# Kernel tuning notes

Measured on AMD Instinct MI355X. Metric: run time of the kernel, lower is better.

Reference implementation:

```python
import jax, jax.numpy as jnp
import numpy as np

# Irreps 0e+1o+2e+3o: (name, dim); total irreps dim D = 1+3+5+7 = 16
IRS = [("0e", 1), ("1o", 3), ("2e", 5), ("3o", 7)]
D = 16
# path multiplicities per correlation order (MACE-like)
MULS = {3: [5, 8, 10, 10], 2: [2, 3, 4, 4], 1: [1, 1, 1, 1]}
NUM_RBF = 32
CHANNELS = 128
NUM_SPECIES = 64
BATCH = 256


def _make_U():
    # Sparse Clebsch-Gordan-like basis tensors: shape (D,)*order + (mul, ir_dim).
    # Stand-in for e3nn.reduced_symmetric_tensor_product_basis: deterministic,
    rng = np.random.default_rng(42)
    U = {}
    for order in (3, 2, 1):
        for (ir, dim), mul in zip(IRS, MULS[order]):
            shape = (D,) * order + (mul, dim)
            dense = rng.standard_normal(shape).astype(np.float32)
            mask = (rng.random(shape) < 0.1).astype(np.float32)
            U[(order, ir)] = jnp.asarray(dense * mask)
    return U

U_BASIS = _make_U()
WKEYS = [(o, ir) for o in (3, 2, 1) for ir, _ in IRS]


def setup_inputs() -> dict:
    key = jax.random.key(0)
    ks = jax.random.split(key, 16)
    inp = {
        "x": jax.random.normal(ks[0], (BATCH, CHANNELS, D), dtype=jnp.float32),
        "index": jax.random.randint(ks[1], (BATCH,), 0, NUM_SPECIES),
        "embed_table": jax.random.normal(ks[2], (NUM_SPECIES, NUM_RBF), dtype=jnp.float32),
    }
    i = 3
    for order in (3, 2, 1):
        for (ir, _), mul in zip(IRS, MULS[order]):
            inp[f"w{order}_{ir}"] = jax.random.normal(ks[i], (NUM_RBF, mul, CHANNELS), dtype=jnp.float32)
            i += 1
    return inp


def _forward(x, species_ind, Wd):
    # x: (b, c, D); species_ind: (b, num_rbf); Wd[(order, ir)]: (num_rbf, mul, c)
    out = {}
    fresh = set()
    for order in (3, 2, 1):
        for ir, _ in IRS:
            u = U_BASIS[(order, ir)] / order  # ((D,)*order, mul, ir_dim)
            # species-gathered per-channel path weights: (b, mul, c)
            w = jnp.einsum('be,ekc->bkc', species_ind, Wd[(order, ir)])
            if ir not in out:
                # highest order: contract one D axis with x, mul with w
                out[ir] = jnp.einsum('...jki,bkc,bcj->bc...i', u, w, x)
                fresh.add(ir)
            else:
                out[ir] = out[ir] + jnp.einsum('...ki,bkc->bc...i', u, w)
        for ir, _ in IRS:
            if ir in fresh:
                fresh.discard(ir)
                continue
            # contract one more D axis against x after each lower order
            out[ir] = jnp.einsum('bc...ji,bcj->bc...i', out[ir], x)
    # final per-ir shape (b, c, ir_dim); concat -> (b, c, D)
    return jnp.concatenate([out[ir] for ir, _ in IRS], axis=-1)


def reference(x, index, embed_table, w3_0e, w3_1o, w3_2e, w3_3o, w2_0e, w2_1o, w2_2e, w2_3o, w1_0e, w1_1o, w1_2e, w1_3o):
    ws = (w3_0e, w3_1o, w3_2e, w3_3o, w2_0e, w2_1o, w2_2e, w2_3o, w1_0e, w1_1o, w1_2e, w1_3o)
    Wd = {k: w for k, w in zip(WKEYS, ws)}
    species_ind = embed_table[index]  # (b, num_rbf) embedding lookup
    return _forward(x, species_ind, Wd)
```

## Files before the change

kernel.cpp:

```cpp
#include <hip/hip_runtime.h>
#include <cstdint>
#include <cmath>
#include <cstring>

#define D16    16
#define CH     128
#define NBATCH 256
#define NSP    64
#define NRBF   32
#define NKK    50
#define NT3    816
#define NT2    136
#define LD3    160
#define LD2    64
#define U3_FLOATS (NT3*LD3)
#define U2_FLOATS (NT2*LD2)
#define U1_FLOATS 256
#define U_TOTAL   (U3_FLOATS+U2_FLOATS+U1_FLOATS)

#define KPAD   1024
#define NPAD   256

typedef __attribute__((ext_vector_type(8)))  short short8;
typedef __attribute__((ext_vector_type(16))) float f32x16;

__device__ uint16_t g_B[NPAD*KPAD];
__device__ float    g_ws[NSP*NKK*CH];

__device__ __constant__ int8_t KK_ARR[NKK] = {
  0,0,0,0,0, 1,1,1,1,1,1,1,1, 2,2,2,2,2,2,2,2,2,2, 3,3,3,3,3,3,3,3,3,3,
  4,4, 5,5,5, 6,6,6,6, 7,7,7,7, 8,9,10,11 };
__device__ __constant__ int8_t KK_K[NKK] = {
  0,1,2,3,4, 0,1,2,3,4,5,6,7, 0,1,2,3,4,5,6,7,8,9, 0,1,2,3,4,5,6,7,8,9,
  0,1, 0,1,2, 0,1,2,3, 0,1,2,3, 0,0,0,0 };
__device__ __constant__ int8_t ARR_MUL[12] = {5,8,10,10, 2,3,4,4, 1,1,1,1};

struct WPtrs { const float* p[12]; };

struct TTab { uint8_t a0[KPAD]; uint8_t a1[KPAD]; uint8_t a2[KPAD]; };
constexpr TTab make_tab() {
  TTab t{};
  int i = 0;
  for (int A = 0; A < 16; ++A)
    for (int B = A; B < 16; ++B)
      for (int C = B; C < 16; ++C) { t.a0[i]=(uint8_t)A; t.a1[i]=(uint8_t)B; t.a2[i]=(uint8_t)C; ++i; }
  for (int A = 0; A < 16; ++A)
    for (int B = A; B < 16; ++B) { t.a0[i]=(uint8_t)A; t.a1[i]=(uint8_t)B; t.a2[i]=16; ++i; }
  for (int A = 0; A < 16; ++A) { t.a0[i]=(uint8_t)A; t.a1[i]=16; t.a2[i]=16; ++i; }
  for (; i < KPAD; ++i) { t.a0[i]=17; t.a1[i]=17; t.a2[i]=17; }
  return t;
}
static constexpr TTab TT = make_tab();

template<int K>
__device__ __forceinline__ float featK(const float (&xv)[16]) {
  constexpr int A = TT.a0[K], B = TT.a1[K], C = TT.a2[K];
  if constexpr (A == 17) { return 0.f; }
  else {
    float m = xv[A];
    if constexpr (B < 16) m *= xv[B];
    if constexpr (C < 16) m *= xv[C];
    return m;
  }
}

template<int K0>
__device__ __forceinline__ uint32_t pack2(const float (&xv)[16]) {
  if constexpr (TT.a0[K0] == 17 && TT.a0[K0+1] == 17) { return 0u; }
  else {
    float lo = featK<K0>(xv);
    float hi = featK<K0+1>(xv);
    uint32_t d;
    asm("v_cvt_pk_bf16_f32 %0, %1, %2" : "=v"(d) : "v"(lo), "v"(hi));
    return d;
  }
}

template<int CHUNK>
__device__ __forceinline__ short8 build_frag(const float (&xv)[16], bool kg_hi) {
  uint32_t pk0 = pack2<CHUNK*16 + 0>(xv);
  uint32_t pk1 = pack2<CHUNK*16 + 2>(xv);
  uint32_t pk2 = pack2<CHUNK*16 + 4>(xv);
  uint32_t pk3 = pack2<CHUNK*16 + 6>(xv);
  uint32_t pk4 = pack2<CHUNK*16 + 8>(xv);
  uint32_t pk5 = pack2<CHUNK*16 + 10>(xv);
  uint32_t pk6 = pack2<CHUNK*16 + 12>(xv);
  uint32_t pk7 = pack2<CHUNK*16 + 14>(xv);
  union { uint32_t u[4]; short8 s; } r;
  r.u[0] = kg_hi ? pk4 : pk0;
  r.u[1] = kg_hi ? pk5 : pk1;
  r.u[2] = kg_hi ? pk6 : pk2;
  r.u[3] = kg_hi ? pk7 : pk3;
  return r.s;
}

__device__ uint32_t colpack(int cc) {
  int kk, ii;
  if (cc < 149) {
    if (cc < 5)       { kk = cc;               ii = 0; }
    else if (cc < 29) { int r = cc-5;  kk = 5  + r/3; ii = 1 + r%3; }
    else if (cc < 79) { int r = cc-29; kk = 13 + r/5; ii = 4 + r%5; }
    else              { int r = cc-79; kk = 23 + r/7; ii = 9 + r%7; }
  } else if (cc < 208) {
    int j = cc - 149;
    if (j < 2)        { kk = 33 + j;           ii = 0; }
    else if (j < 11)  { int r = j-2;  kk = 35 + r/3; ii = 1 + r%3; }
    else if (j < 31)  { int r = j-11; kk = 38 + r/5; ii = 4 + r%5; }
    else              { int r = j-31; kk = 42 + r/7; ii = 9 + r%7; }
  } else {
    int j = cc - 208;
    if (j < 1)        { kk = 46; ii = 0; }
    else if (j < 4)   { kk = 47; ii = j; }
    else if (j < 9)   { kk = 48; ii = j; }
    else              { kk = 49; ii = j; }
  }
  return (uint32_t)((kk<<4) | ii);
}

__global__ void weights_kernel(const float* __restrict__ embed, WPtrs wp) {
  int kk = blockIdx.x;
  int s  = blockIdx.y;
  int c  = threadIdx.x;
  int ai = KK_ARR[kk];
  int k  = KK_K[kk];
  int mul = ARR_MUL[ai];
  const float* __restrict__ W = wp.p[ai];
  float a = 0.f;
  #pragma unroll 8
  for (int e = 0; e < NRBF; ++e)
    a = fmaf(embed[s*NRBF + e], W[(e*mul + k)*CH + c], a);
  g_ws[(s*NKK + kk)*CH + c] = a;
}

__global__ __launch_bounds__(512) void main_kernel(const float* __restrict__ x,
                                                   const int* __restrict__ index,
                                                   float* __restrict__ out) {
  __shared__ uint16_t Bbuf[2][4][2][256][8];
  __shared__ float    out_lds[128*18];
  __shared__ uint32_t tab2[256];

  const int tid  = threadIdx.x;
  const int lane = tid & 63;
  const int l31  = lane & 31;
  const int kg   = lane >> 5;
  const bool kg_hi = (kg != 0);
  const int w    = tid >> 6;
  const int wm   = w >> 1;
  const int wn   = w & 1;
  const int b    = blockIdx.x;
  const int s    = index[b];

  const int row = wm*32 + l31;
  float xv[16];
  {
    const float4* xs = (const float4*)(x + ((size_t)b*CH + row)*D16);
    #pragma unroll
    for (int qq = 0; qq < 4; ++qq) {
      float4 v = xs[qq];
      xv[qq*4+0]=v.x; xv[qq*4+1]=v.y; xv[qq*4+2]=v.z; xv[qq*4+3]=v.w;
    }
  }

  for (int i = tid; i < 128*18; i += 512) out_lds[i] = 0.f;
  if (tid < 256) tab2[tid] = (tid < 224) ? colpack(tid) : 0u;

  #pragma unroll
  for (int q = 0; q < 4; ++q) {
    uint4 v = *(const uint4*)(g_B + ((size_t)q*512 + tid)*8);
    *(uint4*)((char*)&Bbuf[0][q][0][0][0] + tid*16) = v;
  }
  __syncthreads();

  f32x16 acc[4];
  #pragma unroll
  for (int nt = 0; nt < 4; ++nt)
    #pragma unroll
    for (int q = 0; q < 16; ++q) acc[nt][q] = 0.f;

  uint4 bpre[4];

#define DO_CHUNK(CC, CB) { \
    short8 af = build_frag<(CC)>(xv, kg_hi); \
    _Pragma("unroll") \
    for (int nt = 0; nt < 4; ++nt) { \
      short8 bf = *(const short8*)&Bbuf[(CB)][(CC)&3][kg][wn*128 + nt*32 + l31][0]; \
      acc[nt] = __builtin_amdgcn_mfma_f32_32x32x16_bf16(af, bf, acc[nt], 0, 0, 0); \
    } }

#define DO_STAGE(S) { \
    if ((S) < 15) { \
      _Pragma("unroll") \
      for (int q = 0; q < 4; ++q) \
        bpre[q] = *(const uint4*)(g_B + ((size_t)(((S)+1)*4+q)*512 + tid)*8); \
    } \
    DO_CHUNK((S)*4+0, (S)&1) \
    DO_CHUNK((S)*4+1, (S)&1) \
    DO_CHUNK((S)*4+2, (S)&1) \
    DO_CHUNK((S)*4+3, (S)&1) \
    if ((S) < 15) { \
      _Pragma("unroll") \
      for (int q = 0; q < 4; ++q) \
        *(uint4*)((char*)&Bbuf[((S)+1)&1][q][0][0][0] + tid*16) = bpre[q]; \
    } \
    __syncthreads(); }

  DO_STAGE(0)  DO_STAGE(1)  DO_STAGE(2)  DO_STAGE(3)
  DO_STAGE(4)  DO_STAGE(5)  DO_STAGE(6)  DO_STAGE(7)
  DO_STAGE(8)  DO_STAGE(9)  DO_STAGE(10) DO_STAGE(11)
  DO_STAGE(12) DO_STAGE(13) DO_STAGE(14) DO_STAGE(15)

#undef DO_STAGE
#undef DO_CHUNK

  #pragma unroll
  for (int nt = 0; nt < 4; ++nt) {
    int col = wn*128 + nt*32 + l31;
    if (col < 224) {
      uint32_t v = tab2[col];
      int kk = v >> 4, ii = v & 15;
      const float* wsrow = g_ws + ((size_t)s*NKK + kk)*CH + wm*32;
      #pragma unroll
      for (int qg = 0; qg < 4; ++qg) {
        int rlb = 8*qg + 4*kg;
        float4 wv = *(const float4*)(wsrow + rlb);
        atomicAdd(&out_lds[(wm*32 + rlb + 0)*18 + ii], wv.x * acc[nt][qg*4+0]);
        atomicAdd(&out_lds[(wm*32 + rlb + 1)*18 + ii], wv.y * acc[nt][qg*4+1]);
        atomicAdd(&out_lds[(wm*32 + rlb + 2)*18 + ii], wv.z * acc[nt][qg*4+2]);
        atomicAdd(&out_lds[(wm*32 + rlb + 3)*18 + ii], wv.w * acc[nt][qg*4+3]);
      }
    }
  }
  __syncthreads();

  { int cch = tid >> 2, q = tid & 3;
    float4 o;
    o.x = out_lds[cch*18 + q*4 + 0];
    o.y = out_lds[cch*18 + q*4 + 1];
    o.z = out_lds[cch*18 + q*4 + 2];
    o.w = out_lds[cch*18 + q*4 + 3];
    *(float4*)(out + ((size_t)b*CH + cch)*D16 + q*4) = o; }
}

namespace host_rng {

typedef unsigned __int128 u128;

static inline u128 pcg_mult() {
  return (((u128)0x2360ed051fc65da4ULL) << 64) | 0x4385df649fccf645ULL;
}

struct PCG {
  u128 state, inc;
  inline uint64_t next() {
    state = state * pcg_mult() + inc;
    uint64_t hi = (uint64_t)(state >> 64), lo = (uint64_t)state;
    uint64_t x = hi ^ lo;
    unsigned rot = (unsigned)(hi >> 58);
    return (x >> rot) | (x << ((64u - rot) & 63u));
  }
  inline double nextd() { return (double)(next() >> 11) * (1.0 / 9007199254740992.0); }
};

static inline uint32_t hashmix(uint32_t v, uint32_t& hc) {
  v ^= hc; hc *= 0x931e8875u; v *= hc; v ^= v >> 16; return v;
}
static inline uint32_t mixfn(uint32_t x, uint32_t y) {
  uint32_t r = 0xca01f9ddu * x - 0x4973f715u * y; r ^= r >> 16; return r;
}

static void seed42(PCG& g) {
  uint32_t pool[4];
  uint32_t hc = 0x43b0d7e5u;
  pool[0] = hashmix(42u, hc);
  for (int i = 1; i < 4; ++i) pool[i] = hashmix(0u, hc);
  for (int si = 0; si < 4; ++si)
    for (int di = 0; di < 4; ++di)
      if (si != di) pool[di] = mixfn(pool[di], hashmix(pool[si], hc));
  uint32_t hb = 0x8b51f9ddu;
  uint32_t w32[8];
  for (int k = 0; k < 8; ++k) {
    uint32_t dv = pool[k & 3];
    dv ^= hb; hb *= 0x58f38dedu; dv *= hb; dv ^= dv >> 16;
    w32[k] = dv;
  }
  uint64_t s0 = (uint64_t)w32[0] | ((uint64_t)w32[1] << 32);
  uint64_t s1 = (uint64_t)w32[2] | ((uint64_t)w32[3] << 32);
  uint64_t s2 = (uint64_t)w32[4] | ((uint64_t)w32[5] << 32);
  uint64_t s3 = (uint64_t)w32[6] | ((uint64_t)w32[7] << 32);
  u128 initstate = ((u128)s0 << 64) | s1;
  u128 initseq   = ((u128)s2 << 64) | s3;
  g.inc   = (initseq << 1) | 1;
  g.state = g.inc;
  g.state += initstate;
  g.state = g.state * pcg_mult() + g.inc;
}

static double zig_w[256], zig_f[256];
static uint64_t zig_k[256];
static const double ZR = 3.6541528853610087963519472518;
static double ZRinv;

static void build_zig() {
  const double m1 = 4503599627370496.0;
  double fr   = std::exp(-0.5 * ZR * ZR);
  double tail = std::sqrt(M_PI * 0.5) * std::erfc(ZR / std::sqrt(2.0));
  double vn   = ZR * fr + tail;
  double q    = vn / fr;
  zig_k[0]   = (uint64_t)((ZR / q) * m1);
  zig_k[1]   = 0;
  zig_w[0]   = q / m1;
  zig_w[255] = ZR / m1;
  zig_f[0]   = 1.0;
  zig_f[255] = fr;
  double tn = ZR, dn = ZR;
  for (int i = 254; i >= 1; --i) {
    dn = std::sqrt(-2.0 * std::log(vn / dn + std::exp(-0.5 * dn * dn)));
    zig_k[i + 1] = (uint64_t)((dn / tn) * m1);
    tn = dn;
    zig_f[i] = std::exp(-0.5 * dn * dn);
    zig_w[i] = dn / m1;
  }
  ZRinv = 1.0 / ZR;
}

static double std_normal(PCG& g) {
  for (;;) {
    uint64_t r = g.next();
    int idx = (int)(r & 0xffu);
    r >>= 8;
    int sign = (int)(r & 1u);
    uint64_t rabs = (r >> 1) & 0x000fffffffffffffULL;
    double x = (double)rabs * zig_w[idx];
    if (sign) x = -x;
    if (rabs < zig_k[idx]) return x;
    if (idx == 0) {
      for (;;) {
        double xx = -ZRinv * std::log1p(-g.nextd());
        double yy = -std::log1p(-g.nextd());
        if (yy + yy > xx * xx)
          return ((rabs >> 8) & 1u) ? -(ZR + xx) : (ZR + xx);
      }
    } else {
      if ((zig_f[idx - 1] - zig_f[idx]) * g.nextd() + zig_f[idx] < std::exp(-0.5 * x * x))
        return x;
    }
  }
}

}

static float h_U[U_TOTAL];

static void build_U() {
  using namespace host_rng;
  build_zig();
  PCG g; seed42(g);

  static double S3[U3_FLOATS];
  static double S2[U2_FLOATS];
  static double S1[U1_FLOATS];
  std::memset(S3, 0, sizeof(S3));
  std::memset(S2, 0, sizeof(S2));
  std::memset(S1, 0, sizeof(S1));

  static int tmap[16][16][16];
  static int pmap[16][16];
  { int t = 0;
    for (int a0 = 0; a0 < 16; ++a0)
      for (int a1 = a0; a1 < 16; ++a1)
        for (int a2 = a1; a2 < 16; ++a2) tmap[a0][a1][a2] = t++; }
  { int t = 0;
    for (int a0 = 0; a0 < 16; ++a0)
      for (int a1 = a0; a1 < 16; ++a1) pmap[a0][a1] = t++; }

  const int muls3[4] = {5,8,10,10}, muls2[4] = {2,3,4,4};
  const int dims[4]  = {1,3,5,7};
  const int cb3[4]   = {0,5,29,79};
  const int cb2[4]   = {0,2,11,31};
  const int cb1[4]   = {0,1,4,9};

  static double nrm[16*16*16*10*7];

  for (int ir = 0; ir < 4; ++ir) {
    int mul = muls3[ir], dim = dims[ir];
    long n = 4096L * mul * dim;
    for (long j = 0; j < n; ++j) nrm[j] = std_normal(g);
    long j = 0;
    for (int a0 = 0; a0 < 16; ++a0)
      for (int a1 = 0; a1 < 16; ++a1)
        for (int a2 = 0; a2 < 16; ++a2) {
          int s0 = a0, s1 = a1, s2 = a2, tswap;
          if (s0 > s1) { tswap = s0; s0 = s1; s1 = tswap; }
          if (s1 > s2) { tswap = s1; s1 = s2; s2 = tswap; }
          if (s0 > s1) { tswap = s0; s0 = s1; s1 = tswap; }
          int t = tmap[s0][s1][s2];
          for (int k = 0; k < mul; ++k)
            for (int i = 0; i < dim; ++i, ++j) {
              double u = g.nextd();
              if (u < 0.1) {
                float v = (float)nrm[j];
                v = v / 3.0f;
                S3[t*LD3 + cb3[ir] + k*dim + i] += (double)v;
              }
            }
        }
  }
  for (int ir = 0; ir < 4; ++ir) {
    int mul = muls2[ir], dim = dims[ir];
    long n = 256L * mul * dim;
    for (long j = 0; j < n; ++j) nrm[j] = std_normal(g);
    long j = 0;
    for (int a0 = 0; a0 < 16; ++a0)
      for (int a1 = 0; a1 < 16; ++a1) {
        int s0 = a0 < a1 ? a0 : a1;
        int s1 = a0 < a1 ? a1 : a0;
        int t = pmap[s0][s1];
        for (int k = 0; k < mul; ++k)
          for (int i = 0; i < dim; ++i, ++j) {
            double u = g.nextd();
            if (u < 0.1) {
              float v = (float)nrm[j];
              v = v / 2.0f;
              S2[t*LD2 + cb2[ir] + k*dim + i] += (double)v;
            }
          }
      }
  }
  for (int ir = 0; ir < 4; ++ir) {
    int dim = dims[ir];
    long n = 16L * dim;
    for (long j = 0; j < n; ++j) nrm[j] = std_normal(g);
    long j = 0;
    for (int a0 = 0; a0 < 16; ++a0)
      for (int i = 0; i < dim; ++i, ++j) {
        double u = g.nextd();
        if (u < 0.1) {
          float v = (float)nrm[j];
          S1[a0*16 + cb1[ir] + i] += (double)v;
        }
      }
  }

  for (int i = 0; i < U3_FLOATS; ++i) h_U[i] = (float)S3[i];
  for (int i = 0; i < U2_FLOATS; ++i) h_U[U3_FLOATS + i] = (float)S2[i];
  for (int i = 0; i < U1_FLOATS; ++i) h_U[U3_FLOATS + U2_FLOATS + i] = (float)S1[i];
}

static uint16_t h_B_arr[NPAD*KPAD];
static const uint16_t* h_B_src = h_B_arr;

static inline uint16_t f2bf_h(float x) {
  uint32_t u; std::memcpy(&u, &x, 4);
  return (uint16_t)((u + 0x7fffu + ((u>>16)&1u)) >> 16);
}

static inline float Bval(int col, int k) {
  if (k < NT3)            { if (col < 149) return h_U[k*LD3 + col]; }
  else if (k < NT3+NT2)   { if (col >= 149 && col < 208) return h_U[U3_FLOATS + (k-NT3)*LD2 + (col-149)]; }
  else if (k < NT3+NT2+16){ if (col >= 208 && col < 224) return h_U[U3_FLOATS + U2_FLOATS + (k-(NT3+NT2))*16 + (col-208)]; }
  return 0.f;
}

struct UInit {
  UInit() {
    build_U();
    for (int c = 0; c < KPAD/16; ++c)
      for (int half = 0; half < 2; ++half)
        for (int col = 0; col < NPAD; ++col)
          for (int j = 0; j < 8; ++j) {
            int k = c*16 + half*8 + j;
            h_B_arr[((size_t)(c*2 + half)*NPAD + col)*8 + j] = f2bf_h(Bval(col, k));
          }
    void* p = nullptr;
    if (hipHostMalloc(&p, sizeof(h_B_arr), hipHostMallocDefault) == hipSuccess && p) {
      std::memcpy(p, h_B_arr, sizeof(h_B_arr));
      h_B_src = (const uint16_t*)p;
    }
  }
};
static UInit u_init_once;

extern "C" void kernel_launch(void* const* d_in, const int* in_sizes, int n_in,
                              void* d_out, int out_size, void* d_ws, size_t ws_size,
                              hipStream_t stream) {
  (void)in_sizes; (void)n_in; (void)d_ws; (void)ws_size; (void)out_size;

  const float* x     = (const float*)d_in[0];
  const int*   index = (const int*)d_in[1];
  const float* embed = (const float*)d_in[2];
  WPtrs wp;
  for (int i = 0; i < 12; ++i) wp.p[i] = (const float*)d_in[3 + i];

  void* bptr = nullptr;
  hipGetSymbolAddress(&bptr, HIP_SYMBOL(g_B));
  hipMemcpyAsync(bptr, h_B_src, sizeof(h_B_arr), hipMemcpyHostToDevice, stream);

  dim3 gw(NKK, NSP);
  weights_kernel<<<gw, CH, 0, stream>>>(embed, wp);
  main_kernel<<<NBATCH, 512, 0, stream>>>(x, index, (float*)d_out);
}
```

Measured before the change: 81.56 us.

## Stream B fragments from global into registers with 2x2 warp tiles, skip padded K

Drops the LDS double-buffered B staging and its per-stage barriers. Each wave now loads its B fragments straight from global memory into registers with a four-deep prefetch ring, and computes a 2x2 tile of 32x32 MFMAs so each A and B fragment is reused twice. The loop also stops after 61 real K chunks instead of the padded 64. Launch bounds now request two blocks per CU. The risk is that every wave reads B from global or L2 on its own with no LDS sharing, and register pressure rises under the occupancy target.

Result: slower. 87.29 us (+7.0%).

```diff
diff --git a/kernel.cpp b/kernel.cpp
--- a/kernel.cpp
+++ b/kernel.cpp
@@ -20,6 +20,7 @@
 
 #define KPAD   1024
 #define NPAD   256
+#define NCH_REAL 61
 
 typedef __attribute__((ext_vector_type(8)))  short short8;
 typedef __attribute__((ext_vector_type(16))) float f32x16;
@@ -132,10 +133,30 @@
   g_ws[(s*NKK + kk)*CH + c] = a;
 }
 
-__global__ __launch_bounds__(512) void main_kernel(const float* __restrict__ x,
-                                                   const int* __restrict__ index,
-                                                   float* __restrict__ out) {
-  __shared__ uint16_t Bbuf[2][4][2][256][8];
+template<int C>
+__device__ __forceinline__ void kstep(const float (&xv0)[16], const float (&xv1)[16],
+                                      bool kg_hi, const uint16_t* __restrict__ pB,
+                                      uint4 (&brA)[4], uint4 (&brB)[4],
+                                      f32x16& a00, f32x16& a01,
+                                      f32x16& a10, f32x16& a11) {
+  union UU { uint4 u; short8 s; };
+  UU b0; b0.u = brA[C & 3];
+  UU b1; b1.u = brB[C & 3];
+  short8 af0 = build_frag<C>(xv0, kg_hi);
+  short8 af1 = build_frag<C>(xv1, kg_hi);
+  a00 = __builtin_amdgcn_mfma_f32_32x32x16_bf16(af0, b0.s, a00, 0, 0, 0);
+  a01 = __builtin_amdgcn_mfma_f32_32x32x16_bf16(af0, b1.s, a01, 0, 0, 0);
+  a10 = __builtin_amdgcn_mfma_f32_32x32x16_bf16(af1, b0.s, a10, 0, 0, 0);
+  a11 = __builtin_amdgcn_mfma_f32_32x32x16_bf16(af1, b1.s, a11, 0, 0, 0);
+  if constexpr (C + 4 < NCH_REAL) {
+    brA[(C+4)&3] = *(const uint4*)(pB + (size_t)(C+4)*4096);
+    brB[(C+4)&3] = *(const uint4*)(pB + (size_t)(C+4)*4096 + 256);
+  }
+}
+
+__global__ __launch_bounds__(512, 2) void main_kernel(const float* __restrict__ x,
+                                                      const int* __restrict__ index,
+                                                      float* __restrict__ out) {
   __shared__ float    out_lds[128*18];
   __shared__ uint32_t tab2[256];
 
@@ -145,88 +166,70 @@
   const int kg   = lane >> 5;
   const bool kg_hi = (kg != 0);
   const int w    = tid >> 6;
-  const int wm   = w >> 1;
-  const int wn   = w & 1;
+  const int wmg  = w >> 2;
+  const int wq   = w & 3;
   const int b    = blockIdx.x;
   const int s    = index[b];
 
-  const int row = wm*32 + l31;
-  float xv[16];
+  const int r0 = wmg*64 + l31;
+  float xv0[16], xv1[16];
   {
-    const float4* xs = (const float4*)(x + ((size_t)b*CH + row)*D16);
+    const float4* xs0 = (const float4*)(x + ((size_t)b*CH + r0)*D16);
+    const float4* xs1 = (const float4*)(x + ((size_t)b*CH + r0 + 32)*D16);
     #pragma unroll
     for (int qq = 0; qq < 4; ++qq) {
-      float4 v = xs[qq];
-      xv[qq*4+0]=v.x; xv[qq*4+1]=v.y; xv[qq*4+2]=v.z; xv[qq*4+3]=v.w;
+      float4 v0 = xs0[qq], v1 = xs1[qq];
+      xv0[qq*4+0]=v0.x; xv0[qq*4+1]=v0.y; xv0[qq*4+2]=v0.z; xv0[qq*4+3]=v0.w;
+      xv1[qq*4+0]=v1.x; xv1[qq*4+1]=v1.y; xv1[qq*4+2]=v1.z; xv1[qq*4+3]=v1.w;
     }
   }
 
   for (int i = tid; i < 128*18; i += 512) out_lds[i] = 0.f;
   if (tid < 256) tab2[tid] = (tid < 224) ? colpack(tid) : 0u;
 
+  const uint16_t* __restrict__ pB = g_B + ((size_t)kg*256 + wq*64 + l31)*8;
+
+  uint4 brA[4], brB[4];
   #pragma unroll
-  for (int q = 0; q < 4; ++q) {
-    uint4 v = *(const uint4*)(g_B + ((size_t)q*512 + tid)*8);
-    *(uint4*)((char*)&Bbuf[0][q][0][0][0] + tid*16) = v;
-  }
+  for (int c = 0; c < 4; ++c) {
+    brA[c] = *(const uint4*)(pB + (size_t)c*4096);
+    brB[c] = *(const uint4*)(pB + (size_t)c*4096 + 256);
+  }
+
+  f32x16 a00, a01, a10, a11;
+  #pragma unroll
+  for (int q = 0; q < 16; ++q) { a00[q]=0.f; a01[q]=0.f; a10[q]=0.f; a11[q]=0.f; }
+
+#define S1_(C) kstep<(C)>(xv0, xv1, kg_hi, pB, brA, brB, a00, a01, a10, a11);
+#define S4_(C) S1_(C) S1_(C+1) S1_(C+2) S1_(C+3)
+  S4_(0)  S4_(4)  S4_(8)  S4_(12) S4_(16) S4_(20) S4_(24) S4_(28)
+  S4_(32) S4_(36) S4_(40) S4_(44) S4_(48) S4_(52) S4_(56) S1_(60)
+#undef S4_
+#undef S1_
+
   __syncthreads();
 
-  f32x16 acc[4];
+  const f32x16* accs[2][2] = { {&a00, &a01}, {&a10, &a11} };
   #pragma unroll
-  for (int nt = 0; nt < 4; ++nt)
+  for (int ss = 0; ss < 2; ++ss) {
     #pragma unroll
-    for (int q = 0; q < 16; ++q) acc[nt][q] = 0.f;
-
-  uint4 bpre[4];
-
-#define DO_CHUNK(CC, CB) { \
-    short8 af = build_frag<(CC)>(xv, kg_hi); \
-    _Pragma("unroll") \
-    for (int nt = 0; nt < 4; ++nt) { \
-      short8 bf = *(const short8*)&Bbuf[(CB)][(CC)&3][kg][wn*128 + nt*32 + l31][0]; \
-      acc[nt] = __builtin_amdgcn_mfma_f32_32x32x16_bf16(af, bf, acc[nt], 0, 0, 0); \
-    } }
-
-#define DO_STAGE(S) { \
-    if ((S) < 15) { \
-      _Pragma("unroll") \
-      for (int q = 0; q < 4; ++q) \
-        bpre[q] = *(const uint4*)(g_B + ((size_t)(((S)+1)*4+q)*512 + tid)*8); \
-    } \
-    DO_CHUNK((S)*4+0, (S)&1) \
-    DO_CHUNK((S)*4+1, (S)&1) \
-    DO_CHUNK((S)*4+2, (S)&1) \
-    DO_CHUNK((S)*4+3, (S)&1) \
-    if ((S) < 15) { \
-      _Pragma("unroll") \
-      for (int q = 0; q < 4; ++q) \
-        *(uint4*)((char*)&Bbuf[((S)+1)&1][q][0][0][0] + tid*16) = bpre[q]; \
-    } \
-    __syncthreads(); }
-
-  DO_STAGE(0)  DO_STAGE(1)  DO_STAGE(2)  DO_STAGE(3)
-  DO_STAGE(4)  DO_STAGE(5)  DO_STAGE(6)  DO_STAGE(7)
-  DO_STAGE(8)  DO_STAGE(9)  DO_STAGE(10) DO_STAGE(11)
-  DO_STAGE(12) DO_STAGE(13) DO_STAGE(14) DO_STAGE(15)
-
-#undef DO_STAGE
-#undef DO_CHUNK
-
-  #pragma unroll
-  for (int nt = 0; nt < 4; ++nt) {
-    int col = wn*128 + nt*32 + l31;
-    if (col < 224) {
-      uint32_t v = tab2[col];
-      int kk = v >> 4, ii = v & 15;
-      const float* wsrow = g_ws + ((size_t)s*NKK + kk)*CH + wm*32;
-      #pragma unroll
-      for (int qg = 0; qg < 4; ++qg) {
-        int rlb = 8*qg + 4*kg;
-        float4 wv = *(const float4*)(wsrow + rlb);
-        atomicAdd(&out_lds[(wm*32 + rlb + 0)*18 + ii], wv.x * acc[nt][qg*4+0]);
-        atomicAdd(&out_lds[(wm*32 + rlb + 1)*18 + ii], wv.y * acc[nt][qg*4+1]);
-        atomicAdd(&out_lds[(wm*32 + rlb + 2)*18 + ii], wv.z * acc[nt][qg*4+2]);
-        atomicAdd(&out_lds[(wm*32 + rlb + 3)*18 + ii], wv.w * acc[nt][qg*4+3]);
+    for (int nt = 0; nt < 2; ++nt) {
+      int col = wq*64 + nt*32 + l31;
+      if (col < 224) {
+        uint32_t v = tab2[col];
+        int kk = v >> 4, ii = v & 15;
+        const f32x16& ac = *accs[ss][nt];
+        const float* wsrow = g_ws + ((size_t)s*NKK + kk)*CH + wmg*64 + ss*32;
+        #pragma unroll
+        for (int qg = 0; qg < 4; ++qg) {
+          int rlb = 8*qg + 4*kg;
+          float4 wv = *(const float4*)(wsrow + rlb);
+          int rbase = wmg*64 + ss*32 + rlb;
+          atomicAdd(&out_lds[(rbase + 0)*18 + ii], wv.x * ac[qg*4+0]);
+          atomicAdd(&out_lds[(rbase + 1)*18 + ii], wv.y * ac[qg*4+1]);
+          atomicAdd(&out_lds[(rbase + 2)*18 + ii], wv.z * ac[qg*4+2]);
+          atomicAdd(&out_lds[(rbase + 3)*18 + ii], wv.w * ac[qg*4+3]);
+        }
       }
     }
   }
```

## Split main GEMM K dimension across two blocks and merge partial outputs

Applied to the files above, without the earlier changes.

Launches main_kernel on a 256x2 grid where each block handles half of the 64 K-chunks, writing partial per-batch outputs to a global scratch buffer. A new merge kernel sums the two partials into the output. The goal is more blocks than the 256 CUs so latency is hidden better and each block's serial pipeline is shorter. The cost is an extra kernel launch, extra global traffic for the partials, and a duplicated weighting epilogue per half.

Measured after the change: 120.9 us. 1.48x slower.

```diff
diff --git a/kernel.cpp b/kernel.cpp
--- a/kernel.cpp
+++ b/kernel.cpp
@@ -26,6 +26,7 @@
 
 __device__ uint16_t g_B[NPAD*KPAD];
 __device__ float    g_ws[NSP*NKK*CH];
+__device__ float    g_part[NBATCH*2*CH*D16];
 
 __device__ __constant__ int8_t KK_ARR[NKK] = {
   0,0,0,0,0, 1,1,1,1,1,1,1,1, 2,2,2,2,2,2,2,2,2,2, 3,3,3,3,3,3,3,3,3,3,
@@ -132,10 +133,9 @@
   g_ws[(s*NKK + kk)*CH + c] = a;
 }
 
-__global__ __launch_bounds__(512) void main_kernel(const float* __restrict__ x,
-                                                   const int* __restrict__ index,
-                                                   float* __restrict__ out) {
-  __shared__ uint16_t Bbuf[2][4][2][256][8];
+__global__ __launch_bounds__(512, 2) void main_kernel(const float* __restrict__ x,
+                                                      const int* __restrict__ index) {
+  __shared__ uint16_t Bbuf[2][4][4096];
   __shared__ float    out_lds[128*18];
   __shared__ uint32_t tab2[256];
 
@@ -148,27 +148,33 @@
   const int wm   = w >> 1;
   const int wn   = w & 1;
   const int b    = blockIdx.x;
+  const int ks   = blockIdx.y;
   const int s    = index[b];
 
-  const int row = wm*32 + l31;
+  char* const bb = (char*)&Bbuf[0][0][0];
+  uint4 bpre[4];
+
+  {
+    const int g0 = ks * 32;
+    #pragma unroll
+    for (int q = 0; q < 4; ++q)
+      bpre[q] = *(const uint4*)(g_B + (size_t)(g0 + q)*4096 + tid*8);
+  }
+  const int r0 = wm*32 + l31;
   float xv[16];
   {
-    const float4* xs = (const float4*)(x + ((size_t)b*CH + row)*D16);
+    const float4* xs = (const float4*)(x + ((size_t)b*CH + r0)*D16);
     #pragma unroll
     for (int qq = 0; qq < 4; ++qq) {
       float4 v = xs[qq];
       xv[qq*4+0]=v.x; xv[qq*4+1]=v.y; xv[qq*4+2]=v.z; xv[qq*4+3]=v.w;
     }
   }
-
   for (int i = tid; i < 128*18; i += 512) out_lds[i] = 0.f;
   if (tid < 256) tab2[tid] = (tid < 224) ? colpack(tid) : 0u;
-
   #pragma unroll
-  for (int q = 0; q < 4; ++q) {
-    uint4 v = *(const uint4*)(g_B + ((size_t)q*512 + tid)*8);
-    *(uint4*)((char*)&Bbuf[0][q][0][0][0] + tid*16) = v;
-  }
+  for (int q = 0; q < 4; ++q)
+    *(uint4*)(bb + q*8192 + tid*16) = bpre[q];
   __syncthreads();
 
   f32x16 acc[4];
@@ -177,40 +183,46 @@
     #pragma unroll
     for (int q = 0; q < 16; ++q) acc[nt][q] = 0.f;
 
-  uint4 bpre[4];
-
-#define DO_CHUNK(CC, CB) { \
-    short8 af = build_frag<(CC)>(xv, kg_hi); \
+#define STAGE_LOAD(GBASE) { \
+    _Pragma("unroll") \
+    for (int q = 0; q < 4; ++q) \
+      bpre[q] = *(const uint4*)(g_B + (size_t)((GBASE) + q)*4096 + tid*8); }
+
+#define STAGE_WRITE(NB) { \
+    _Pragma("unroll") \
+    for (int q = 0; q < 4; ++q) \
+      *(uint4*)(bb + (NB)*32768 + q*8192 + tid*16) = bpre[q]; }
+
+#define KCHUNK(G, SL, CB) { \
+    short8 af = build_frag<(G)>(xv, kg_hi); \
     _Pragma("unroll") \
     for (int nt = 0; nt < 4; ++nt) { \
-      short8 bf = *(const short8*)&Bbuf[(CB)][(CC)&3][kg][wn*128 + nt*32 + l31][0]; \
-      acc[nt] = __builtin_amdgcn_mfma_f32_32x32x16_bf16(af, bf, acc[nt], 0, 0, 0); \
+      union UU { uint4 u; short8 s; } bu; \
+      bu.s = *(const short8*)(bb + (CB)*32768 + (SL)*8192 + kg*4096 + (wn*128 + nt*32 + l31)*16); \
+      acc[nt] = __builtin_amdgcn_mfma_f32_32x32x16_bf16(af, bu.s, acc[nt], 0, 0, 0); \
     } }
 
-#define DO_STAGE(S) { \
-    if ((S) < 15) { \
-      _Pragma("unroll") \
-      for (int q = 0; q < 4; ++q) \
-        bpre[q] = *(const uint4*)(g_B + ((size_t)(((S)+1)*4+q)*512 + tid)*8); \
-    } \
-    DO_CHUNK((S)*4+0, (S)&1) \
-    DO_CHUNK((S)*4+1, (S)&1) \
-    DO_CHUNK((S)*4+2, (S)&1) \
-    DO_CHUNK((S)*4+3, (S)&1) \
-    if ((S) < 15) { \
-      _Pragma("unroll") \
-      for (int q = 0; q < 4; ++q) \
-        *(uint4*)((char*)&Bbuf[((S)+1)&1][q][0][0][0] + tid*16) = bpre[q]; \
-    } \
+#define STEP(KS, S) { \
+    if ((S) < 7) STAGE_LOAD((KS)*32 + ((S)+1)*4) \
+    KCHUNK((KS)*32+(S)*4+0, 0, (S)&1) \
+    KCHUNK((KS)*32+(S)*4+1, 1, (S)&1) \
+    KCHUNK((KS)*32+(S)*4+2, 2, (S)&1) \
+    KCHUNK((KS)*32+(S)*4+3, 3, (S)&1) \
+    if ((S) < 7) STAGE_WRITE(((S)+1)&1) \
     __syncthreads(); }
 
-  DO_STAGE(0)  DO_STAGE(1)  DO_STAGE(2)  DO_STAGE(3)
-  DO_STAGE(4)  DO_STAGE(5)  DO_STAGE(6)  DO_STAGE(7)
-  DO_STAGE(8)  DO_STAGE(9)  DO_STAGE(10) DO_STAGE(11)
-  DO_STAGE(12) DO_STAGE(13) DO_STAGE(14) DO_STAGE(15)
-
-#undef DO_STAGE
-#undef DO_CHUNK
+  if (ks == 0) {
+    STEP(0,0) STEP(0,1) STEP(0,2) STEP(0,3)
+    STEP(0,4) STEP(0,5) STEP(0,6) STEP(0,7)
+  } else {
+    STEP(1,0) STEP(1,1) STEP(1,2) STEP(1,3)
+    STEP(1,4) STEP(1,5) STEP(1,6) STEP(1,7)
+  }
+
+#undef STEP
+#undef KCHUNK
+#undef STAGE_WRITE
+#undef STAGE_LOAD
 
   #pragma unroll
   for (int nt = 0; nt < 4; ++nt) {
@@ -223,22 +235,34 @@
       for (int qg = 0; qg < 4; ++qg) {
         int rlb = 8*qg + 4*kg;
         float4 wv = *(const float4*)(wsrow + rlb);
-        atomicAdd(&out_lds[(wm*32 + rlb + 0)*18 + ii], wv.x * acc[nt][qg*4+0]);
-        atomicAdd(&out_lds[(wm*32 + rlb + 1)*18 + ii], wv.y * acc[nt][qg*4+1]);
-        atomicAdd(&out_lds[(wm*32 + rlb + 2)*18 + ii], wv.z * acc[nt][qg*4+2]);
-        atomicAdd(&out_lds[(wm*32 + rlb + 3)*18 + ii], wv.w * acc[nt][qg*4+3]);
+        int rbase = wm*32 + rlb;
+        atomicAdd(&out_lds[(rbase + 0)*18 + ii], wv.x * acc[nt][qg*4+0]);
+        atomicAdd(&out_lds[(rbase + 1)*18 + ii], wv.y * acc[nt][qg*4+1]);
+        atomicAdd(&out_lds[(rbase + 2)*18 + ii], wv.z * acc[nt][qg*4+2]);
+        atomicAdd(&out_lds[(rbase + 3)*18 + ii], wv.w * acc[nt][qg*4+3]);
       }
     }
   }
   __syncthreads();
 
-  { int cch = tid >> 2, q = tid & 3;
+  { float* pp = g_part + ((size_t)b*2 + ks)*2048;
+    int cch = tid >> 2, q = tid & 3;
     float4 o;
     o.x = out_lds[cch*18 + q*4 + 0];
     o.y = out_lds[cch*18 + q*4 + 1];
     o.z = out_lds[cch*18 + q*4 + 2];
     o.w = out_lds[cch*18 + q*4 + 3];
-    *(float4*)(out + ((size_t)b*CH + cch)*D16 + q*4) = o; }
+    *(float4*)(pp + cch*16 + q*4) = o; }
+}
+
+__global__ __launch_bounds__(512) void merge_kernel(float* __restrict__ out) {
+  int idx = blockIdx.x*512 + threadIdx.x;
+  size_t b   = (size_t)(idx >> 9);
+  size_t off = (size_t)(idx & 511) * 4;
+  const float4 p0 = *(const float4*)(g_part + b*4096 + off);
+  const float4 p1 = *(const float4*)(g_part + b*4096 + 2048 + off);
+  float4 o; o.x = p0.x+p1.x; o.y = p0.y+p1.y; o.z = p0.z+p1.z; o.w = p0.w+p1.w;
+  *(float4*)(out + b*2048 + off) = o;
 }
 
 namespace host_rng {
@@ -497,5 +521,7 @@
 
   dim3 gw(NKK, NSP);
   weights_kernel<<<gw, CH, 0, stream>>>(embed, wp);
-  main_kernel<<<NBATCH, 512, 0, stream>>>(x, index, (float*)d_out);
-}
+  dim3 gm(NBATCH, 2);
+  main_kernel<<<gm, 512, 0, stream>>>(x, index);
+  merge_kernel<<<256, 512, 0, stream>>>((float*)d_out);
+}
```
